# Kernel optimization log

Hardware: AMD Instinct MI355X
Metric: run time of the kernel (lower is better)

## Reference

```python
import jax, jax.numpy as jnp
import numpy as np

B, C, H, W_IMG = 16, 3, 384, 384
P = 16
G = H // P                 # 24
NPATCH = G * G             # 576
SEQ = NPATCH + 1           # 577 (with cls token)
D, FF, NH, NL = 768, 3072, 12, 12
NCLS = 1000
K = int(0.5 * NPATCH)
HD = D // NH
EPS = 1e-6


def _ln(x, g, b):
    mu = jnp.mean(x, axis=-1, keepdims=True)
    var = jnp.mean((x - mu) ** 2, axis=-1, keepdims=True)
    return (x - mu) * jax.lax.rsqrt(var + EPS) * g + b


def setup_inputs() -> dict:
    key = jax.random.key(0)
    ks = jax.random.split(key, 12)
    s = 0.02
    return {
        "x": jax.random.normal(ks[0], (B, C, H, W_IMG), jnp.float32),
        "patch_w": jax.random.normal(ks[1], (D, C, P, P), jnp.float32) * s,
        "patch_b": jnp.zeros((D,), jnp.float32),
        "cls_tok": jax.random.normal(ks[2], (1, 1, D), jnp.float32) * s,
        "pos_emb": jax.random.normal(ks[3], (1, SEQ, D), jnp.float32) * s,
        "ln1_g": jnp.ones((NL, D), jnp.float32),
        "ln1_b": jnp.zeros((NL, D), jnp.float32),
        "Wqkv": jax.random.normal(ks[4], (NL, D, 3 * D), jnp.float32) * s,
        "bqkv": jnp.zeros((NL, 3 * D), jnp.float32),
        "Wo": jax.random.normal(ks[5], (NL, D, D), jnp.float32) * s,
        "bo": jnp.zeros((NL, D), jnp.float32),
        "ln2_g": jnp.ones((NL, D), jnp.float32),
        "ln2_b": jnp.zeros((NL, D), jnp.float32),
        "W1": jax.random.normal(ks[6], (NL, D, FF), jnp.float32) * s,
        "b1": jnp.zeros((NL, FF), jnp.float32),
        "W2": jax.random.normal(ks[7], (NL, FF, D), jnp.float32) * s,
        "b2": jnp.zeros((NL, D), jnp.float32),
        "lnf_g": jnp.ones((D,), jnp.float32),
        "lnf_b": jnp.zeros((D,), jnp.float32),
        "fc_w": jax.random.normal(ks[8], (D, NCLS), jnp.float32) * s,
        "fc_b": jnp.zeros((NCLS,), jnp.float32),
    }


def reference(x, patch_w, patch_b, cls_tok, pos_emb, ln1_g, ln1_b, Wqkv, bqkv,
              Wo, bo, ln2_g, ln2_b, W1, b1, W2, b2, lnf_g, lnf_b, fc_w, fc_b):
    b = x.shape[0]
    # patch embedding: strided conv -> (b, D, G, G) -> (b, NPATCH, D)
    patches = jax.lax.conv_general_dilated(
        x, patch_w, window_strides=(P, P), padding="VALID",
        dimension_numbers=("NCHW", "OIHW", "NCHW")) + patch_b[None, :, None, None]
    tok = patches.reshape(b, D, NPATCH).transpose(0, 2, 1)
    tok = jnp.concatenate([jnp.broadcast_to(cls_tok, (b, 1, D)), tok], axis=1)
    tok = tok + pos_emb  # seq matches original_seq_len, no resize

    # saliency = avg-pool of raw first input channel (net_G output is unused in the source)
    pooled = x[:, 0].reshape(b, G, P, G, P).mean(axis=(2, 4)).reshape(b, NPATCH)
    _, idx = jax.lax.top_k(jnp.abs(pooled), K)          # (b, K)
    spatial = tok[:, 1:, :]
    sel = jnp.take_along_axis(spatial, idx[:, :, None], axis=1)  # (b, K, D)
    h = jnp.concatenate([tok[:, :1, :], sel], axis=1)   # (b, K+1, D)
    S = h.shape[1]

    scale = 1.0 / np.sqrt(HD)
    for i in range(NL):
        y = _ln(h, ln1_g[i], ln1_b[i])
        qkv = y @ Wqkv[i] + bqkv[i]
        q, k_, v = jnp.split(qkv, 3, axis=-1)
        q = q.reshape(b, S, NH, HD)
        k_ = k_.reshape(b, S, NH, HD)
        v = v.reshape(b, S, NH, HD)
        att = jnp.einsum("bqhd,bkhd->bhqk", q, k_) * scale
        att = jax.nn.softmax(att, axis=-1)
        o = jnp.einsum("bhqk,bkhd->bqhd", att, v).reshape(b, S, D)
        h = h + (o @ Wo[i] + bo[i])
        y = _ln(h, ln2_g[i], ln2_b[i])
        h = h + (jax.nn.gelu(y @ W1[i] + b1[i], approximate=False) @ W2[i] + b2[i])

    cls_out = _ln(h, lnf_g, lnf_b)[:, 0]   # pool_type='tok'
    return cls_out @ fc_w + fc_b


if __name__ == "__main__":
    out = reference(**setup_inputs())
    print(out.shape)
```

## Files before the change

kernel.cpp:

```cpp
#include <hip/hip_runtime.h>
#include <hip/hip_bf16.h>
#include <math.h>

#define BB 16
#define SS 289
#define DD 768
#define FFD 3072
#define NHD 12
#define NLAY 12
#define KSEL 288
#define NPATCH 576
#define MNTOT 3551232

typedef short bf16x8 __attribute__((ext_vector_type(8)));
typedef short bf16x4 __attribute__((ext_vector_type(4)));
typedef float f32x4 __attribute__((ext_vector_type(4)));

typedef __attribute__((address_space(3))) void lds_t;
typedef __attribute__((address_space(1))) const void glb_t;

__device__ __forceinline__ void gload16(const void* g, void* l) {
    __builtin_amdgcn_global_load_lds((glb_t*)g, (lds_t*)l, 16, 0, 0);
}

__device__ __forceinline__ bf16x8 ds_read128(unsigned addr) {
    bf16x8 r;
    asm volatile("ds_read_b128 %0, %1" : "=v"(r) : "v"(addr));
    return r;
}

__device__ __forceinline__ float gelu_f(float v) {
    return 0.5f * v * (1.0f + erff(v * 0.70710678118654752f));
}

__device__ __forceinline__ void store_val(float* p, float v) { *p = v; }
__device__ __forceinline__ void store_val(__hip_bfloat16* p, float v) { *p = __float2bfloat16(v); }

__global__ __launch_bounds__(256) void pool_kernel(const float* __restrict__ x,
                                                   float* __restrict__ pooled) {
    int bp = blockIdx.x;
    int b = bp / NPATCH, p = bp - b * NPATCH;
    int gi = p / 24, gj = p - gi * 24;
    int tid = threadIdx.x;
    int pi = tid >> 4, pj = tid & 15;
    float v = x[((size_t)(b * 3) * 384 + gi * 16 + pi) * 384 + gj * 16 + pj];
    #pragma unroll
    for (int o = 32; o > 0; o >>= 1) v += __shfl_down(v, o);
    __shared__ float red[4];
    if ((tid & 63) == 0) red[tid >> 6] = v;
    __syncthreads();
    if (tid == 0) pooled[bp] = (red[0] + red[1] + red[2] + red[3]) * (1.0f / 256.0f);
}

__global__ __launch_bounds__(576) void topk_kernel(const float* __restrict__ pooled,
                                                   int* __restrict__ idxsel) {
    __shared__ float a[NPATCH];
    int b = blockIdx.x, tid = threadIdx.x;
    a[tid] = fabsf(pooled[b * NPATCH + tid]);
    __syncthreads();
    float mine = a[tid];
    int rank = 0;
    for (int j = 0; j < NPATCH; ++j) {
        float aj = a[j];
        rank += (aj > mine) || (aj == mine && j < tid);
    }
    if (rank < KSEL) idxsel[b * KSEL + rank] = tid;
}

__global__ __launch_bounds__(256) void convert_bf16(const float* __restrict__ in,
                                                    __hip_bfloat16* __restrict__ out,
                                                    int n) {
    int i = blockIdx.x * 256 + threadIdx.x;
    if (i < n) out[i] = __float2bfloat16(in[i]);
}

__global__ __launch_bounds__(256) void convert_layer(const float* __restrict__ wqkv,
                                                     const float* __restrict__ wo,
                                                     const float* __restrict__ w1,
                                                     const float* __restrict__ w2,
                                                     __hip_bfloat16* __restrict__ oqkv,
                                                     __hip_bfloat16* __restrict__ owo,
                                                     __hip_bfloat16* __restrict__ ow1,
                                                     __hip_bfloat16* __restrict__ ow2) {
    __shared__ float tb[32][33];
    int bid = blockIdx.x;
    const float* W; __hip_bfloat16* O; int K, N, tile;
    if (bid < 1728)      { W = wqkv; O = oqkv; K = 768;  N = 2304; tile = bid; }
    else if (bid < 2304) { W = wo;   O = owo;  K = 768;  N = 768;  tile = bid - 1728; }
    else if (bid < 4608) { W = w1;   O = ow1;  K = 768;  N = 3072; tile = bid - 2304; }
    else                 { W = w2;   O = ow2;  K = 3072; N = 768;  tile = bid - 4608; }
    int ntx = N >> 5;
    int n0 = (tile % ntx) << 5, k0 = (tile / ntx) << 5;
    int t = threadIdx.x;
    int r = t >> 3, c = (t & 7) << 2;
    float4 v = *(const float4*)&W[(size_t)(k0 + r) * N + n0 + c];
    tb[r][c] = v.x; tb[r][c + 1] = v.y; tb[r][c + 2] = v.z; tb[r][c + 3] = v.w;
    __syncthreads();
    int n = t >> 3, k = (t & 7) << 2;
    __hip_bfloat16* dst = &O[(size_t)(n0 + n) * K + k0 + k];
    __hip_bfloat16 o4[4];
    #pragma unroll
    for (int j = 0; j < 4; ++j) o4[j] = __float2bfloat16(tb[k + j][n]);
    *(bf16x4*)dst = *(const bf16x4*)o4;
}

__global__ __launch_bounds__(256) void im2col_kernel(const float* __restrict__ x,
                                                     const int* __restrict__ idxsel,
                                                     __hip_bfloat16* __restrict__ col) {
    int t = blockIdx.x;
    int b = t / KSEL, r = t - b * KSEL;
    int p = idxsel[b * KSEL + r];
    int gi = p / 24, gj = p - gi * 24;
    int tid = threadIdx.x;
    int pi = tid >> 4, pj = tid & 15;
    __hip_bfloat16* crow = col + (size_t)t * 768;
    #pragma unroll
    for (int c = 0; c < 3; ++c)
        crow[c * 256 + tid] = __float2bfloat16(
            x[((size_t)(b * 3 + c) * 384 + gi * 16 + pi) * 384 + gj * 16 + pj]);
}

__global__ __launch_bounds__(256) void assemble_tokens(const float* __restrict__ temp,
                                                       const float* __restrict__ cls_tok,
                                                       const float* __restrict__ pos_emb,
                                                       const int* __restrict__ idxsel,
                                                       float* __restrict__ h) {
    int row = blockIdx.x;
    int b = row / SS, s = row - b * SS;
    int tid = threadIdx.x;
    float* hrow = h + (size_t)row * DD;
    if (s == 0) {
        #pragma unroll
        for (int c = 0; c < 3; ++c) {
            int j = c * 256 + tid;
            hrow[j] = cls_tok[j] + pos_emb[j];
        }
    } else {
        int r = s - 1;
        int p = idxsel[b * KSEL + r];
        const float* trow = temp + (size_t)(b * KSEL + r) * DD;
        const float* pe = pos_emb + (size_t)(1 + p) * DD;
        #pragma unroll
        for (int c = 0; c < 3; ++c) {
            int j = c * 256 + tid;
            hrow[j] = trow[j] + pe[j];
        }
    }
}

template <typename T>
__global__ __launch_bounds__(256) void ln_kernel(const float* __restrict__ in,
                                                 T* __restrict__ out,
                                                 const float* __restrict__ g,
                                                 const float* __restrict__ be,
                                                 size_t in_stride) {
    int row = blockIdx.x;
    const float* r = in + (size_t)row * in_stride;
    T* w = out + (size_t)row * DD;
    int tid = threadIdx.x;
    float v0 = r[tid], v1 = r[256 + tid], v2 = r[512 + tid];
    float s = v0 + v1 + v2;
    #pragma unroll
    for (int o = 32; o > 0; o >>= 1) s += __shfl_down(s, o);
    __shared__ float red[4];
    if ((tid & 63) == 0) red[tid >> 6] = s;
    __syncthreads();
    float mu = (red[0] + red[1] + red[2] + red[3]) * (1.0f / 768.0f);
    float d0 = v0 - mu, d1 = v1 - mu, d2 = v2 - mu;
    float q = d0 * d0 + d1 * d1 + d2 * d2;
    #pragma unroll
    for (int o = 32; o > 0; o >>= 1) q += __shfl_down(q, o);
    __syncthreads();
    if ((tid & 63) == 0) red[tid >> 6] = q;
    __syncthreads();
    float var = (red[0] + red[1] + red[2] + red[3]) * (1.0f / 768.0f);
    float rs = rsqrtf(var + 1e-6f);
    store_val(&w[tid],       d0 * rs * g[tid]       + be[tid]);
    store_val(&w[256 + tid], d1 * rs * g[256 + tid] + be[256 + tid]);
    store_val(&w[512 + tid], d2 * rs * g[512 + tid] + be[512 + tid]);
}

template <typename OUT_T, int ACT, int RES, int SPLITK>
__global__ __launch_bounds__(512) void gemm_bf16(const __hip_bfloat16* __restrict__ A,
                                                 const __hip_bfloat16* __restrict__ BT,
                                                 OUT_T* __restrict__ C,
                                                 const float* __restrict__ bias,
                                                 const float* __restrict__ res,
                                                 float* __restrict__ part,
                                                 int M, int N, int K) {
    __shared__ __hip_bfloat16 smA[3][128 * 32];
    __shared__ __hip_bfloat16 smB[3][256 * 32];
    const int t = threadIdx.x;
    const int lane = t & 63, wid = t >> 6;
    const int wr = wid >> 2, wc = wid & 3;
    const int l15 = lane & 15, l4 = lane >> 4;

    const int gx = gridDim.x;
    const int nwg = gx * gridDim.y;
    const int orig = blockIdx.y * gx + blockIdx.x;
    const int q8 = nwg >> 3, r8 = nwg & 7;
    const int xcd = orig & 7, linb = orig >> 3;
    const int swz = (xcd < r8 ? xcd * (q8 + 1) : r8 * (q8 + 1) + (xcd - r8) * q8) + linb;
    const int m0 = (swz / gx) << 7;
    const int n0 = (swz - (swz / gx) * gx) << 8;

    const int Ksub = K / SPLITK;
    const int kz0 = blockIdx.z * Ksub;

    int ra[4], rb[4];
    #pragma unroll
    for (int f = 0; f < 4; ++f) {
        int ml = wr * 64 + f * 16 + l15;
        ra[f] = ml * 64 + ((l4 ^ ((ml >> 1) & 3)) << 4);
        int nl = wc * 64 + f * 16 + l15;
        rb[f] = nl * 64 + ((l4 ^ ((nl >> 1) & 3)) << 4);
    }

    size_t aoff, boff[2];
    {
        int mA = t >> 2;
        int kcA = (t & 3) ^ ((mA >> 1) & 3);
        int gmA = m0 + mA; if (gmA > M - 1) gmA = M - 1;
        aoff = (size_t)gmA * K + kz0 + kcA * 8;
        #pragma unroll
        for (int it = 0; it < 2; ++it) {
            int s = it * 512 + t;
            int mB = s >> 2;
            int kc = (s & 3) ^ ((mB >> 1) & 3);
            boff[it] = (size_t)(n0 + mB) * K + kz0 + kc * 8;
        }
    }
    const int wb = wid << 10;
    const unsigned ldsA0 = (unsigned)(size_t)(lds_t*)&smA[0][0];
    const unsigned ldsB0 = (unsigned)(size_t)(lds_t*)&smB[0][0];

    auto STAGE = [&](int kt, int buf) {
        int k0e = kt << 5;
        gload16(A + aoff + k0e,     (char*)(&smA[buf][0]) + wb);
        gload16(BT + boff[0] + k0e, (char*)(&smB[buf][0]) + wb);
        gload16(BT + boff[1] + k0e, (char*)(&smB[buf][0]) + 8192 + wb);
    };

    f32x4 acc[4][4];
    #pragma unroll
    for (int i = 0; i < 4; ++i)
        #pragma unroll
        for (int j = 0; j < 4; ++j) acc[i][j] = (f32x4){0.f, 0.f, 0.f, 0.f};

    const int nt = Ksub >> 5;
    STAGE(0, 0); STAGE(1, 1);
    int cur = 0, stb = 2;
    for (int kt = 0; kt < nt; ++kt) {
        if (kt + 1 < nt) asm volatile("s_waitcnt vmcnt(3)" ::: "memory");
        else             asm volatile("s_waitcnt vmcnt(0)" ::: "memory");
        asm volatile("s_barrier" ::: "memory");
        if (kt + 2 < nt) STAGE(kt + 2, stb);
        const unsigned sa = ldsA0 + cur * 8192u;
        const unsigned sb = ldsB0 + cur * 16384u;
        bf16x8 af[4], bf[4];
        #pragma unroll
        for (int f = 0; f < 4; ++f) {
            af[f] = ds_read128(sa + ra[f]);
            bf[f] = ds_read128(sb + rb[f]);
        }
        asm volatile("s_waitcnt lgkmcnt(0)" ::: "memory");
        __builtin_amdgcn_sched_barrier(0);
        #pragma unroll
        for (int i = 0; i < 4; ++i)
            #pragma unroll
            for (int j = 0; j < 4; ++j)
                acc[i][j] = __builtin_amdgcn_mfma_f32_16x16x32_bf16(af[i], bf[j], acc[i][j], 0, 0, 0);
        cur = cur == 2 ? 0 : cur + 1;
        stb = stb == 2 ? 0 : stb + 1;
    }

    if (SPLITK == 1) {
        #pragma unroll
        for (int i = 0; i < 4; ++i) {
            int gmb = m0 + wr * 64 + i * 16 + l4 * 4;
            #pragma unroll
            for (int j = 0; j < 4; ++j) {
                int gn = n0 + wc * 64 + j * 16 + l15;
                float bv = bias ? bias[gn] : 0.f;
                #pragma unroll
                for (int r = 0; r < 4; ++r) {
                    int gm = gmb + r;
                    if (gm < M) {
                        float v = acc[i][j][r] + bv;
                        if (ACT) v = gelu_f(v);
                        if (RES) v += res[(size_t)gm * N + gn];
                        store_val(&C[(size_t)gm * N + gn], v);
                    }
                }
            }
        }
    } else {
        float* pz = part + (size_t)blockIdx.z * M * N;
        #pragma unroll
        for (int i = 0; i < 4; ++i) {
            int gmb = m0 + wr * 64 + i * 16 + l4 * 4;
            #pragma unroll
            for (int j = 0; j < 4; ++j) {
                int gn = n0 + wc * 64 + j * 16 + l15;
                #pragma unroll
                for (int r = 0; r < 4; ++r) {
                    int gm = gmb + r;
                    if (gm < M) pz[(size_t)gm * N + gn] = acc[i][j][r];
                }
            }
        }
    }
}

template <int NPART>
__global__ __launch_bounds__(256) void combine_res(const float* __restrict__ part,
                                                   const float* __restrict__ bias,
                                                   float* __restrict__ h,
                                                   int MN, int N) {
    int i = (blockIdx.x * 256 + threadIdx.x) * 4;
    if (i >= MN) return;
    float4 v = *(const float4*)&part[i];
    #pragma unroll
    for (int z = 1; z < NPART; ++z) {
        float4 p = *(const float4*)&part[(size_t)z * MN + i];
        v.x += p.x; v.y += p.y; v.z += p.z; v.w += p.w;
    }
    int n = i % N;
    float4 bv = *(const float4*)&bias[n];
    float4 hv = *(const float4*)&h[i];
    v.x += bv.x + hv.x; v.y += bv.y + hv.y; v.z += bv.z + hv.z; v.w += bv.w + hv.w;
    *(float4*)&h[i] = v;
}

template <int NPART>
__global__ __launch_bounds__(256) void combine_ln(const float* __restrict__ part,
                                                  const float* __restrict__ bias,
                                                  float* __restrict__ h,
                                                  const float* __restrict__ g,
                                                  const float* __restrict__ be,
                                                  __hip_bfloat16* __restrict__ out) {
    int row = blockIdx.x, tid = threadIdx.x;
    size_t base = (size_t)row * DD;
    float a[3];
    #pragma unroll
    for (int k = 0; k < 3; ++k) {
        int j = k * 256 + tid;
        float s = part[base + j];
        #pragma unroll
        for (int z = 1; z < NPART; ++z) s += part[(size_t)z * MNTOT + base + j];
        s += bias[j] + h[base + j];
        h[base + j] = s;
        a[k] = s;
    }
    float s = a[0] + a[1] + a[2];
    #pragma unroll
    for (int o = 32; o > 0; o >>= 1) s += __shfl_down(s, o);
    __shared__ float red[4];
    if ((tid & 63) == 0) red[tid >> 6] = s;
    __syncthreads();
    float mu = (red[0] + red[1] + red[2] + red[3]) * (1.0f / 768.0f);
    float d0 = a[0] - mu, d1 = a[1] - mu, d2 = a[2] - mu;
    float q = d0 * d0 + d1 * d1 + d2 * d2;
    #pragma unroll
    for (int o = 32; o > 0; o >>= 1) q += __shfl_down(q, o);
    __syncthreads();
    if ((tid & 63) == 0) red[tid >> 6] = q;
    __syncthreads();
    float var = (red[0] + red[1] + red[2] + red[3]) * (1.0f / 768.0f);
    float rs = rsqrtf(var + 1e-6f);
    out[base + tid]       = __float2bfloat16(d0 * rs * g[tid]       + be[tid]);
    out[base + 256 + tid] = __float2bfloat16(d1 * rs * g[256 + tid] + be[256 + tid]);
    out[base + 512 + tid] = __float2bfloat16(d2 * rs * g[512 + tid] + be[512 + tid]);
}

__global__ __launch_bounds__(256) void head_gemm(const float* __restrict__ yf,
                                                 const float* __restrict__ fc_w,
                                                 const float* __restrict__ fc_b,
                                                 float* __restrict__ out) {
    __shared__ float part[128];
    const int tid = threadIdx.x;
    const int nl = tid & 127, kh = tid >> 7;
    const int m = blockIdx.y;
    const int n = blockIdx.x * 128 + nl;
    float acc = 0.f;
    if (n < 1000) {
        const float* yr = yf + (size_t)m * 768 + kh * 384;
        const float* wp = fc_w + (size_t)kh * 384 * 1000 + n;
        #pragma unroll 4
        for (int k = 0; k < 384; ++k)
            acc = fmaf(yr[k], wp[(size_t)k * 1000], acc);
    }
    if (kh == 1) part[nl] = acc;
    __syncthreads();
    if (kh == 0 && n < 1000)
        out[(size_t)m * 1000 + n] = acc + part[nl] + fc_b[n];
}

__global__ __launch_bounds__(64) void attn_fused(const __hip_bfloat16* __restrict__ qkv,
                                                 __hip_bfloat16* __restrict__ o) {
    __shared__ __hip_bfloat16 p_lds[32][40];
    __shared__ __hip_bfloat16 v_lds[32][68];
    const int qt = blockIdx.x, bh = blockIdx.y;
    const int b = bh / NHD, hd = bh - b * NHD;
    const int lane = threadIdx.x;
    const int l15 = lane & 15, l4 = lane >> 4;
    const size_t tb = (size_t)b * SS;
    const int hc = hd * 64;

    bf16x8 aq[2][2];
    #pragma unroll
    for (int qi = 0; qi < 2; ++qi) {
        int qr = qt * 32 + qi * 16 + l15;
        if (qr >= SS) qr = SS - 1;
        const __hip_bfloat16* qrow = qkv + (tb + qr) * 2304 + hc;
        #pragma unroll
        for (int kd = 0; kd < 2; ++kd)
            aq[qi][kd] = *(const bf16x8*)(qrow + kd * 32 + l4 * 8);
    }

    float m_run[2][4], l_run[2][4];
    f32x4 oa[2][4];
    #pragma unroll
    for (int qi = 0; qi < 2; ++qi)
        #pragma unroll
        for (int r = 0; r < 4; ++r) { m_run[qi][r] = -1e30f; l_run[qi][r] = 0.f; }
    #pragma unroll
    for (int qi = 0; qi < 2; ++qi)
        #pragma unroll
        for (int dt = 0; dt < 4; ++dt) oa[qi][dt] = (f32x4){0.f, 0.f, 0.f, 0.f};

    for (int kt = 0; kt < 10; ++kt) {
        const int kbase = kt * 32;
        bf16x4 vreg[8];
        #pragma unroll
        for (int it = 0; it < 8; ++it) {
            int vr = kbase + it * 4 + l4;
            if (vr >= SS) vr = SS - 1;
            vreg[it] = *(const bf16x4*)(qkv + (tb + vr) * 2304 + 1536 + hc + l15 * 4);
        }
        bf16x8 bk[2][2];
        #pragma unroll
        for (int ki = 0; ki < 2; ++ki) {
            int kr = kbase + ki * 16 + l15;
            if (kr >= SS) kr = SS - 1;
            const __hip_bfloat16* krow = qkv + (tb + kr) * 2304 + 768 + hc;
            #pragma unroll
            for (int kd = 0; kd < 2; ++kd)
                bk[ki][kd] = *(const bf16x8*)(krow + kd * 32 + l4 * 8);
        }
        f32x4 s[2][2];
        #pragma unroll
        for (int qi = 0; qi < 2; ++qi)
            #pragma unroll
            for (int ki = 0; ki < 2; ++ki) {
                f32x4 a = (f32x4){0.f, 0.f, 0.f, 0.f};
                #pragma unroll
                for (int kd = 0; kd < 2; ++kd)
                    a = __builtin_amdgcn_mfma_f32_16x16x32_bf16(aq[qi][kd], bk[ki][kd], a, 0, 0, 0);
                s[qi][ki] = a;
            }
        #pragma unroll
        for (int ki = 0; ki < 2; ++ki) {
            bool valid = (kbase + ki * 16 + l15) < SS;
            #pragma unroll
            for (int qi = 0; qi < 2; ++qi)
                #pragma unroll
                for (int r = 0; r < 4; ++r)
                    s[qi][ki][r] = valid ? s[qi][ki][r] * 0.125f : -1e30f;
        }
        float p[2][2][4];
        #pragma unroll
        for (int qi = 0; qi < 2; ++qi) {
            float tm[4];
            #pragma unroll
            for (int r = 0; r < 4; ++r) tm[r] = fmaxf(s[qi][0][r], s[qi][1][r]);
            #pragma unroll
            for (int sh = 1; sh < 16; sh <<= 1)
                #pragma unroll
                for (int r = 0; r < 4; ++r) tm[r] = fmaxf(tm[r], __shfl_xor(tm[r], sh));
            float rs[4];
            #pragma unroll
            for (int r = 0; r < 4; ++r) {
                float mn = fmaxf(m_run[qi][r], tm[r]);
                float corr = __expf(m_run[qi][r] - mn);
                m_run[qi][r] = mn;
                float p0 = __expf(s[qi][0][r] - mn);
                float p1 = __expf(s[qi][1][r] - mn);
                p[qi][0][r] = p0; p[qi][1][r] = p1;
                rs[r] = p0 + p1;
                l_run[qi][r] *= corr;
                #pragma unroll
                for (int dt = 0; dt < 4; ++dt) oa[qi][dt][r] *= corr;
            }
            #pragma unroll
            for (int sh = 1; sh < 16; sh <<= 1)
                #pragma unroll
                for (int r = 0; r < 4; ++r) rs[r] += __shfl_xor(rs[r], sh);
            #pragma unroll
            for (int r = 0; r < 4; ++r) l_run[qi][r] += rs[r];
        }
        #pragma unroll
        for (int qi = 0; qi < 2; ++qi)
            #pragma unroll
            for (int ki = 0; ki < 2; ++ki)
                #pragma unroll
                for (int r = 0; r < 4; ++r)
                    p_lds[qi * 16 + l4 * 4 + r][ki * 16 + l15] = __float2bfloat16(p[qi][ki][r]);
        #pragma unroll
        for (int it = 0; it < 8; ++it)
            *(bf16x4*)&v_lds[it * 4 + l4][l15 * 4] = vreg[it];
        __syncthreads();
        bf16x8 pa[2];
        #pragma unroll
        for (int qi = 0; qi < 2; ++qi)
            pa[qi] = *(const bf16x8*)&p_lds[qi * 16 + l15][l4 * 8];
        bf16x8 vb[4];
        #pragma unroll
        for (int dt = 0; dt < 4; ++dt) {
            bf16x8 v;
            #pragma unroll
            for (int j = 0; j < 8; ++j)
                v[j] = *(const short*)&v_lds[l4 * 8 + j][dt * 16 + l15];
            vb[dt] = v;
        }
        #pragma unroll
        for (int qi = 0; qi < 2; ++qi)
            #pragma unroll
            for (int dt = 0; dt < 4; ++dt)
                oa[qi][dt] = __builtin_amdgcn_mfma_f32_16x16x32_bf16(pa[qi], vb[dt], oa[qi][dt], 0, 0, 0);
        __syncthreads();
    }
    #pragma unroll
    for (int qi = 0; qi < 2; ++qi)
        #pragma unroll
        for (int r = 0; r < 4; ++r) {
            int q = qt * 32 + qi * 16 + l4 * 4 + r;
            if (q < SS) {
                float inv = 1.0f / l_run[qi][r];
                __hip_bfloat16* orow = o + (tb + q) * 768 + hc;
                #pragma unroll
                for (int dt = 0; dt < 4; ++dt)
                    orow[dt * 16 + l15] = __float2bfloat16(oa[qi][dt][r] * inv);
            }
        }
}

static const size_t OFF_POOLED = 0;
static const size_t OFF_IDX    = 10240;
static const size_t OFF_H      = 16384;
static const size_t OFF_YB     = 3567616;
static const size_t OFF_OB     = 5343232;
static const size_t OFF_QKVB   = 7118848;
static const size_t OFF_WBUF   = 12445696;
static const size_t OFF_PWB    = 15984640;
static const size_t OFF_YF     = 16279552;
static const size_t OFF_BIG    = 16291840;
static const size_t OFF_PART   = 23394304;

extern "C" void kernel_launch(void* const* d_in, const int* in_sizes, int n_in,
                              void* d_out, int out_size, void* d_ws, size_t ws_size,
                              hipStream_t stream) {
    const float* x       = (const float*)d_in[0];
    const float* patch_w = (const float*)d_in[1];
    const float* patch_b = (const float*)d_in[2];
    const float* cls_tok = (const float*)d_in[3];
    const float* pos_emb = (const float*)d_in[4];
    const float* ln1_g   = (const float*)d_in[5];
    const float* ln1_b   = (const float*)d_in[6];
    const float* Wqkv    = (const float*)d_in[7];
    const float* bqkv    = (const float*)d_in[8];
    const float* Wo      = (const float*)d_in[9];
    const float* bo      = (const float*)d_in[10];
    const float* ln2_g   = (const float*)d_in[11];
    const float* ln2_b   = (const float*)d_in[12];
    const float* W1      = (const float*)d_in[13];
    const float* b1      = (const float*)d_in[14];
    const float* W2      = (const float*)d_in[15];
    const float* b2      = (const float*)d_in[16];
    const float* lnf_g   = (const float*)d_in[17];
    const float* lnf_b   = (const float*)d_in[18];
    const float* fc_w    = (const float*)d_in[19];
    const float* fc_b    = (const float*)d_in[20];
    float* out = (float*)d_out;
    float* ws  = (float*)d_ws;

    float*          pooled = ws + OFF_POOLED;
    int*            idxsel = (int*)(ws + OFF_IDX);
    float*          h      = ws + OFF_H;
    __hip_bfloat16* yb     = (__hip_bfloat16*)(ws + OFF_YB);
    __hip_bfloat16* ob     = (__hip_bfloat16*)(ws + OFF_OB);
    __hip_bfloat16* qkvb   = (__hip_bfloat16*)(ws + OFF_QKVB);
    __hip_bfloat16* wbuf   = (__hip_bfloat16*)(ws + OFF_WBUF);
    __hip_bfloat16* pwb    = (__hip_bfloat16*)(ws + OFF_PWB);
    float*          yf     = ws + OFF_YF;
    float*          big    = ws + OFF_BIG;
    float*          part   = ws + OFF_PART;
    __hip_bfloat16* col    = (__hip_bfloat16*)big;
    float*          temp   = big + 1769472;
    __hip_bfloat16* hidden = (__hip_bfloat16*)big;

    __hip_bfloat16* wqkvT = wbuf;
    __hip_bfloat16* woT   = wbuf + 1769472;
    __hip_bfloat16* w1T   = wbuf + 2359296;
    __hip_bfloat16* w2T   = wbuf + 4718592;

    const int M = BB * SS;
    const int MG = 37;
    const int MN = M * DD;

    pool_kernel<<<BB * NPATCH, 256, 0, stream>>>(x, pooled);
    topk_kernel<<<BB, 576, 0, stream>>>(pooled, idxsel);
    convert_bf16<<<(589824 + 255) / 256, 256, 0, stream>>>(patch_w, pwb, 589824);
    im2col_kernel<<<BB * KSEL, 256, 0, stream>>>(x, idxsel, col);
    gemm_bf16<float, 0, 0, 1><<<dim3(3, 36), 512, 0, stream>>>(
        col, pwb, temp, patch_b, nullptr, nullptr, 4608, DD, DD);
    assemble_tokens<<<BB * SS, 256, 0, stream>>>(temp, cls_tok, pos_emb, idxsel, h);

    ln_kernel<__hip_bfloat16><<<M, 256, 0, stream>>>(h, yb, ln1_g, ln1_b, DD);

    for (int i = 0; i < NLAY; ++i) {
        convert_layer<<<6912, 256, 0, stream>>>(Wqkv + (size_t)i * DD * 3 * DD,
                                                Wo + (size_t)i * DD * DD,
                                                W1 + (size_t)i * DD * FFD,
                                                W2 + (size_t)i * FFD * DD,
                                                wqkvT, woT, w1T, w2T);

        gemm_bf16<__hip_bfloat16, 0, 0, 1><<<dim3(9, MG), 512, 0, stream>>>(
            yb, wqkvT, qkvb, bqkv + (size_t)i * 3 * DD, nullptr, nullptr, M, 3 * DD, DD);
        attn_fused<<<dim3(10, BB * NHD), 64, 0, stream>>>(qkvb, ob);
        gemm_bf16<float, 0, 0, 2><<<dim3(3, MG, 2), 512, 0, stream>>>(
            ob, woT, (float*)nullptr, nullptr, nullptr, part, M, DD, DD);
        combine_ln<2><<<M, 256, 0, stream>>>(part, bo + (size_t)i * DD, h,
                                             ln2_g + (size_t)i * DD, ln2_b + (size_t)i * DD, yb);
        gemm_bf16<__hip_bfloat16, 1, 0, 1><<<dim3(12, MG), 512, 0, stream>>>(
            yb, w1T, hidden, b1 + (size_t)i * FFD, nullptr, nullptr, M, FFD, DD);
        gemm_bf16<float, 0, 0, 4><<<dim3(3, MG, 4), 512, 0, stream>>>(
            hidden, w2T, (float*)nullptr, nullptr, nullptr, part, M, DD, FFD);
        if (i + 1 < NLAY)
            combine_ln<4><<<M, 256, 0, stream>>>(part, b2 + (size_t)i * DD, h,
                                                 ln1_g + (size_t)(i + 1) * DD,
                                                 ln1_b + (size_t)(i + 1) * DD, yb);
        else
            combine_res<4><<<(MN / 4 + 255) / 256, 256, 0, stream>>>(
                part, b2 + (size_t)i * DD, h, MN, DD);
    }

    ln_kernel<float><<<BB, 256, 0, stream>>>(h, yf, lnf_g, lnf_b, (size_t)SS * DD);
    head_gemm<<<dim3(8, 16), 256, 0, stream>>>(yf, fc_w, fc_b, out);
}
```

Before: 2.351 ms.

## Compute only the CLS row in the final transformer layer

Only the CLS token of the last layer reaches the output, so the final layer now computes K/V for all tokens but runs attention for just the first query block. The Wo, LN2, MLP and final LN steps run only on the 16 CLS rows, using a new small fp32 GEMV-style kernel that reads the fp32 weights directly. The final layer converts only Wqkv to bf16, skipping conversion of Wo, W1 and W2. This removes most of the last layer's GEMM and weight-conversion work, but relies on attn_fused with grid x=1 covering query row 0.

```diff
diff --git a/kernel.cpp b/kernel.cpp
--- a/kernel.cpp
+++ b/kernel.cpp
@@ -35,6 +35,8 @@
 
 __device__ __forceinline__ void store_val(float* p, float v) { *p = v; }
 __device__ __forceinline__ void store_val(__hip_bfloat16* p, float v) { *p = __float2bfloat16(v); }
+__device__ __forceinline__ float load_f(const float* p) { return *p; }
+__device__ __forceinline__ float load_f(const __hip_bfloat16* p) { return __bfloat162float(*p); }
 
 __global__ __launch_bounds__(256) void pool_kernel(const float* __restrict__ x,
                                                    float* __restrict__ pooled) {
@@ -72,6 +74,26 @@
                                                     int n) {
     int i = blockIdx.x * 256 + threadIdx.x;
     if (i < n) out[i] = __float2bfloat16(in[i]);
+}
+
+__global__ __launch_bounds__(256) void convert_w(const float* __restrict__ W,
+                                                 __hip_bfloat16* __restrict__ O,
+                                                 int K, int N) {
+    __shared__ float tb[32][33];
+    int ntx = N >> 5;
+    int tile = blockIdx.x;
+    int n0 = (tile % ntx) << 5, k0 = (tile / ntx) << 5;
+    int t = threadIdx.x;
+    int r = t >> 3, c = (t & 7) << 2;
+    float4 v = *(const float4*)&W[(size_t)(k0 + r) * N + n0 + c];
+    tb[r][c] = v.x; tb[r][c + 1] = v.y; tb[r][c + 2] = v.z; tb[r][c + 3] = v.w;
+    __syncthreads();
+    int n = t >> 3, k = (t & 7) << 2;
+    __hip_bfloat16* dst = &O[(size_t)(n0 + n) * K + k0 + k];
+    __hip_bfloat16 o4[4];
+    #pragma unroll
+    for (int j = 0; j < 4; ++j) o4[j] = __float2bfloat16(tb[k + j][n]);
+    *(bf16x4*)dst = *(const bf16x4*)o4;
 }
 
 __global__ __launch_bounds__(256) void convert_layer(const float* __restrict__ wqkv,
@@ -313,26 +335,6 @@
 }
 
 template <int NPART>
-__global__ __launch_bounds__(256) void combine_res(const float* __restrict__ part,
-                                                   const float* __restrict__ bias,
-                                                   float* __restrict__ h,
-                                                   int MN, int N) {
-    int i = (blockIdx.x * 256 + threadIdx.x) * 4;
-    if (i >= MN) return;
-    float4 v = *(const float4*)&part[i];
-    #pragma unroll
-    for (int z = 1; z < NPART; ++z) {
-        float4 p = *(const float4*)&part[(size_t)z * MN + i];
-        v.x += p.x; v.y += p.y; v.z += p.z; v.w += p.w;
-    }
-    int n = i % N;
-    float4 bv = *(const float4*)&bias[n];
-    float4 hv = *(const float4*)&h[i];
-    v.x += bv.x + hv.x; v.y += bv.y + hv.y; v.z += bv.z + hv.z; v.w += bv.w + hv.w;
-    *(float4*)&h[i] = v;
-}
-
-template <int NPART>
 __global__ __launch_bounds__(256) void combine_ln(const float* __restrict__ part,
                                                   const float* __restrict__ bias,
                                                   float* __restrict__ h,
@@ -371,6 +373,38 @@
     out[base + tid]       = __float2bfloat16(d0 * rs * g[tid]       + be[tid]);
     out[base + 256 + tid] = __float2bfloat16(d1 * rs * g[256 + tid] + be[256 + tid]);
     out[base + 512 + tid] = __float2bfloat16(d2 * rs * g[512 + tid] + be[512 + tid]);
+}
+
+template <typename AT, int ACT, int RES>
+__global__ __launch_bounds__(512) void small_gemm(const AT* __restrict__ A, size_t a_str,
+                                                  const float* __restrict__ W,
+                                                  const float* __restrict__ bias,
+                                                  const float* __restrict__ res, size_t r_str,
+                                                  float* __restrict__ out, int N, int K) {
+    __shared__ float alds[3072];
+    __shared__ float red[4][128];
+    const int tid = threadIdx.x;
+    const int nl = tid & 127, kq = tid >> 7;
+    const int m = blockIdx.y;
+    const int n = blockIdx.x * 128 + nl;
+    for (int i = tid; i < K; i += 512) alds[i] = load_f(&A[(size_t)m * a_str + i]);
+    __syncthreads();
+    float acc = 0.f;
+    const int kc = K >> 2;
+    if (n < N) {
+        const float* wp = W + (size_t)kq * kc * N + n;
+        const float* ap = alds + kq * kc;
+        for (int k = 0; k < kc; ++k)
+            acc = fmaf(ap[k], wp[(size_t)k * N], acc);
+    }
+    red[kq][nl] = acc;
+    __syncthreads();
+    if (kq == 0 && n < N) {
+        float v = red[0][nl] + red[1][nl] + red[2][nl] + red[3][nl] + bias[n];
+        if (ACT) v = gelu_f(v);
+        if (RES) v += res[(size_t)m * r_str + n];
+        out[(size_t)m * N + n] = v;
+    }
 }
 
 __global__ __launch_bounds__(256) void head_gemm(const float* __restrict__ yf,
@@ -556,6 +590,7 @@
 static const size_t OFF_YF     = 16279552;
 static const size_t OFF_BIG    = 16291840;
 static const size_t OFF_PART   = 23394304;
+static const size_t OFF_SMALL  = 37599232;
 
 extern "C" void kernel_launch(void* const* d_in, const int* in_sizes, int n_in,
                               void* d_out, int out_size, void* d_ws, size_t ws_size,
@@ -595,6 +630,7 @@
     float*          yf     = ws + OFF_YF;
     float*          big    = ws + OFF_BIG;
     float*          part   = ws + OFF_PART;
+    float*          sm     = ws + OFF_SMALL;
     __hip_bfloat16* col    = (__hip_bfloat16*)big;
     float*          temp   = big + 1769472;
     __hip_bfloat16* hidden = (__hip_bfloat16*)big;
@@ -604,9 +640,13 @@
     __hip_bfloat16* w1T   = wbuf + 2359296;
     __hip_bfloat16* w2T   = wbuf + 4718592;
 
+    float* h_cls   = sm;
+    float* y_cls   = sm + 12288;
+    float* hid_cls = sm + 24576;
+    float* hfin    = sm + 73728;
+
     const int M = BB * SS;
     const int MG = 37;
-    const int MN = M * DD;
 
     pool_kernel<<<BB * NPATCH, 256, 0, stream>>>(x, pooled);
     topk_kernel<<<BB, 576, 0, stream>>>(pooled, idxsel);
@@ -618,7 +658,7 @@
 
     ln_kernel<__hip_bfloat16><<<M, 256, 0, stream>>>(h, yb, ln1_g, ln1_b, DD);
 
-    for (int i = 0; i < NLAY; ++i) {
+    for (int i = 0; i < NLAY - 1; ++i) {
         convert_layer<<<6912, 256, 0, stream>>>(Wqkv + (size_t)i * DD * 3 * DD,
                                                 Wo + (size_t)i * DD * DD,
                                                 W1 + (size_t)i * DD * FFD,
@@ -636,15 +676,30 @@
             yb, w1T, hidden, b1 + (size_t)i * FFD, nullptr, nullptr, M, FFD, DD);
         gemm_bf16<float, 0, 0, 4><<<dim3(3, MG, 4), 512, 0, stream>>>(
             hidden, w2T, (float*)nullptr, nullptr, nullptr, part, M, DD, FFD);
-        if (i + 1 < NLAY)
-            combine_ln<4><<<M, 256, 0, stream>>>(part, b2 + (size_t)i * DD, h,
-                                                 ln1_g + (size_t)(i + 1) * DD,
-                                                 ln1_b + (size_t)(i + 1) * DD, yb);
-        else
-            combine_res<4><<<(MN / 4 + 255) / 256, 256, 0, stream>>>(
-                part, b2 + (size_t)i * DD, h, MN, DD);
-    }
-
-    ln_kernel<float><<<BB, 256, 0, stream>>>(h, yf, lnf_g, lnf_b, (size_t)SS * DD);
+        combine_ln<4><<<M, 256, 0, stream>>>(part, b2 + (size_t)i * DD, h,
+                                             ln1_g + (size_t)(i + 1) * DD,
+                                             ln1_b + (size_t)(i + 1) * DD, yb);
+    }
+
+    {
+        const int L = NLAY - 1;
+        convert_w<<<72 * 24, 256, 0, stream>>>(Wqkv + (size_t)L * DD * 3 * DD, wqkvT, DD, 3 * DD);
+        gemm_bf16<__hip_bfloat16, 0, 0, 1><<<dim3(9, MG), 512, 0, stream>>>(
+            yb, wqkvT, qkvb, bqkv + (size_t)L * 3 * DD, nullptr, nullptr, M, 3 * DD, DD);
+        attn_fused<<<dim3(1, BB * NHD), 64, 0, stream>>>(qkvb, ob);
+        small_gemm<__hip_bfloat16, 0, 1><<<dim3(6, 16), 512, 0, stream>>>(
+            ob, (size_t)SS * DD, Wo + (size_t)L * DD * DD, bo + (size_t)L * DD,
+            h, (size_t)SS * DD, h_cls, DD, DD);
+        ln_kernel<float><<<16, 256, 0, stream>>>(h_cls, y_cls, ln2_g + (size_t)L * DD,
+                                                 ln2_b + (size_t)L * DD, DD);
+        small_gemm<float, 1, 0><<<dim3(24, 16), 512, 0, stream>>>(
+            y_cls, DD, W1 + (size_t)L * DD * FFD, b1 + (size_t)L * FFD,
+            nullptr, 0, hid_cls, FFD, DD);
+        small_gemm<float, 0, 1><<<dim3(6, 16), 512, 0, stream>>>(
+            hid_cls, FFD, W2 + (size_t)L * FFD * DD, b2 + (size_t)L * DD,
+            h_cls, DD, hfin, DD, FFD);
+    }
+
+    ln_kernel<float><<<16, 256, 0, stream>>>(hfin, yf, lnf_g, lnf_b, DD);
     head_gemm<<<dim3(8, 16), 256, 0, stream>>>(yf, fc_w, fc_b, out);
 }
```

Measured after the change: 2.368 ms. Within noise of the previous version (+0.8%).
